# Performance work log

Measured on AMD Instinct MI355X. Metric: run time of the kernel, lower is better.

The kernel has to match this reference:

```python
import jax, jax.numpy as jnp
import numpy as np

B, T, S = 32, 64, 256
H, E, V = 512, 256, 32000
NH = 8
HD = H // NH  # 64
L = 2  # gru layers
SCALE = float(np.sqrt(HD))


def setup_inputs() -> dict:
    key = jax.random.key(0)
    ks = jax.random.split(key, 32)

    def rn(k, shape, s=0.02):
        return (jax.random.normal(k, shape) * s).astype(jnp.float32)

    inp = {}
    inp["tgt"] = jax.random.randint(ks[0], (B, T), 0, V)
    inp["encoder_out"] = jax.random.normal(ks[1], (B, S, H), dtype=jnp.float32)
    inp["decoder_init"] = jax.random.normal(ks[2], (B, H), dtype=jnp.float32)
    inp["src_mask"] = jnp.ones((B, S), dtype=jnp.int32)
    # parameters
    inp["emb_table"] = rn(ks[3], (V, E)).at[0].set(0.0)  # padding_idx=0
    inp["w_ep"] = rn(ks[4], (H, E)); inp["b_ep"] = jnp.zeros((H,), jnp.float32)
    inp["wq"] = rn(ks[5], (H, H)); inp["bq"] = jnp.zeros((H,), jnp.float32)
    inp["wk"] = rn(ks[6], (H, H)); inp["bk"] = jnp.zeros((H,), jnp.float32)
    inp["wv"] = rn(ks[7], (H, H)); inp["bv"] = jnp.zeros((H,), jnp.float32)
    inp["wo"] = rn(ks[8], (H, H)); inp["bo"] = jnp.zeros((H,), jnp.float32)
    # GRU layer 0: input 2H, layer 1: input H
    inp["w_ih0"] = rn(ks[9], (3 * H, 2 * H)); inp["w_hh0"] = rn(ks[10], (3 * H, H))
    inp["b_ih0"] = jnp.zeros((3 * H,), jnp.float32); inp["b_hh0"] = jnp.zeros((3 * H,), jnp.float32)
    inp["w_ih1"] = rn(ks[11], (3 * H, H)); inp["w_hh1"] = rn(ks[12], (3 * H, H))
    inp["b_ih1"] = jnp.zeros((3 * H,), jnp.float32); inp["b_hh1"] = jnp.zeros((3 * H,), jnp.float32)
    # output MLP
    inp["w_o1"] = rn(ks[13], (H, 2 * H)); inp["b_o1"] = jnp.zeros((H,), jnp.float32)
    inp["w_o2"] = rn(ks[14], (V, H)); inp["b_o2"] = jnp.zeros((V,), jnp.float32)
    return inp


def _gru_cell(x, h, w_ih, w_hh, b_ih, b_hh):
    gi = x @ w_ih.T + b_ih
    gh = h @ w_hh.T + b_hh
    i_r, i_z, i_n = jnp.split(gi, 3, axis=-1)
    h_r, h_z, h_n = jnp.split(gh, 3, axis=-1)
    r = jax.nn.sigmoid(i_r + h_r)
    z = jax.nn.sigmoid(i_z + h_z)
    n = jnp.tanh(i_n + r * h_n)
    return (1.0 - z) * n + z * h


def reference(tgt, encoder_out, decoder_init, src_mask,
              emb_table, w_ep, b_ep, wq, bq, wk, bk, wv, bv, wo, bo,
              w_ih0, w_hh0, b_ih0, b_hh0, w_ih1, w_hh1, b_ih1, b_hh1,
              w_o1, b_o1, w_o2, b_o2):
    # initial hidden: [L, B, H], clamped
    hidden0 = jnp.clip(jnp.broadcast_to(decoder_init[None], (L, B, H)), -10.0, 10.0)
    # K/V projections of encoder_out are step-invariant -> hoist out of the loop
    Kh = jnp.clip(encoder_out @ wk.T + bk, -100.0, 100.0).reshape(B, S, NH, HD)
    Vh = (encoder_out @ wv.T + bv).reshape(B, S, NH, HD)
    pad = (src_mask == 0)  # [B, S]

    def step(hidden, tok):
        emb = emb_table[tok] @ w_ep.T + b_ep                      # [B, H]
        q = jnp.clip(hidden[-1] @ wq.T + bq, -100.0, 100.0).reshape(B, NH, HD)
        scores = jnp.einsum('bhd,bshd->bhs', q, Kh) / SCALE       # [B, NH, S]
        scores = jnp.where(pad[:, None, :], -10000.0, scores)
        attn = jax.nn.softmax(scores, axis=-1)
        ctx = jnp.einsum('bhs,bshd->bhd', attn, Vh).reshape(B, H)
        ctx = jnp.clip(ctx @ wo.T + bo, -100.0, 100.0)            # [B, H]
        x = jnp.concatenate([emb, ctx], axis=1)                   # [B, 2H]
        h0 = _gru_cell(x, hidden[0], w_ih0, w_hh0, b_ih0, b_hh0)
        h1 = _gru_cell(h0, hidden[1], w_ih1, w_hh1, b_ih1, b_hh1)
        new_hidden = jnp.clip(jnp.stack([h0, h1]), -10.0, 10.0)
        comb = jnp.concatenate([h1, ctx], axis=1)                 # gru_out pre-clamp
        out = jax.nn.relu(comb @ w_o1.T + b_o1) @ w_o2.T + b_o2   # [B, V]
        return new_hidden, jnp.clip(out, -100.0, 100.0)

    # teacher forcing (tf_ratio = 1.0): input at step t is tgt[:, t-1]
    _, outs = jax.lax.scan(step, hidden0, tgt[:, :-1].T)          # [T-1, B, V]
    outputs = jnp.concatenate(
        [jnp.zeros((B, 1, V), outs.dtype), outs.transpose(1, 0, 2)], axis=1)
    return outputs
```

## Files before the change

kernel.cpp:

```cpp
#include <hip/hip_runtime.h>
#include <hip/hip_bf16.h>
#include <math.h>

#define B 32
#define T 64
#define S 256
#define H 512
#define E 256
#define V 32000
#define NH 8
#define HD 64
#define TS 63
#define NR 2016
#define G3 1536

typedef short bf16x8 __attribute__((ext_vector_type(8)));
typedef float f32x4 __attribute__((ext_vector_type(4)));

__device__ __forceinline__ unsigned short f2bf(float f) {
    union { float f; unsigned u; } v; v.f = f;
    unsigned r = v.u + 0x7FFF + ((v.u >> 16) & 1);
    return (unsigned short)(r >> 16);
}
__device__ __forceinline__ float clipf(float v, float lo, float hi) {
    return fminf(hi, fmaxf(lo, v));
}
__device__ __forceinline__ float sigf(float x) { return 1.0f / (1.0f + __expf(-x)); }

__device__ __forceinline__ void stA(float* p, float v) {
    __hip_atomic_store(p, v, __ATOMIC_RELAXED, __HIP_MEMORY_SCOPE_AGENT);
}
__device__ __forceinline__ unsigned long long ldA64(const void* p) {
    return __hip_atomic_load((const unsigned long long*)p, __ATOMIC_RELAXED, __HIP_MEMORY_SCOPE_AGENT);
}

#define XIDX(k) ((((k) >> 7) * 132) + ((k) & 127))
#define BLP 528


__global__ void k_zero_t0(float* out) {
    int idx = blockIdx.x * 256 + threadIdx.x;
    int n = B * V / 4;
    if (idx < n) {
        int b = idx / (V / 4);
        int v4 = idx % (V / 4);
        float4* p = (float4*)(out + (size_t)b * T * V) + v4;
        *p = make_float4(0.f, 0.f, 0.f, 0.f);
    }
}

__global__ void k_init_h(const float* dec, float* h0n, float* h1s) {
    int i = blockIdx.x * 256 + threadIdx.x;
    if (i < B * H) {
        float v = clipf(dec[i], -10.f, 10.f);
        h0n[16384 + i] = v;
        h1s[16384 + i] = v;
    }
}

__global__ __launch_bounds__(256) void k_kv(const float* __restrict__ enc,
        const float* __restrict__ wk, const float* __restrict__ bk,
        const float* __restrict__ wv, const float* __restrict__ bv,
        float* __restrict__ kht, float* __restrict__ vh) {
    __shared__ float x[8][512];
    int r0 = blockIdx.x * 8;
    for (int idx = threadIdx.x; idx < 4096; idx += 256) {
        int rr = idx >> 9, k = idx & 511;
        x[rr][k] = enc[(size_t)(r0 + rr) * 512 + k];
    }
    __syncthreads();
    int b = r0 >> 8, s0 = r0 & 255;
    for (int ii = 0; ii < 2; ++ii) {
        int i = threadIdx.x + ii * 256;
        const float* wkr = wk + (size_t)i * 512;
        const float* wvr = wv + (size_t)i * 512;
        float aK[8], aV[8];
        float bk0 = bk[i], bv0 = bv[i];
        #pragma unroll
        for (int rr = 0; rr < 8; ++rr) { aK[rr] = bk0; aV[rr] = bv0; }
        for (int k = 0; k < 512; k += 4) {
            float4 a = *(const float4*)(wkr + k);
            float4 c = *(const float4*)(wvr + k);
            #pragma unroll
            for (int rr = 0; rr < 8; ++rr) {
                float4 xv = *(const float4*)(&x[rr][k]);
                aK[rr] += a.x*xv.x + a.y*xv.y + a.z*xv.z + a.w*xv.w;
                aV[rr] += c.x*xv.x + c.y*xv.y + c.z*xv.z + c.w*xv.w;
            }
        }
        #pragma unroll
        for (int rr = 0; rr < 8; ++rr) {
            kht[((size_t)b * 512 + i) * 256 + s0 + rr] = clipf(aK[rr], -100.f, 100.f);
            vh[((size_t)b * 256 + s0 + rr) * 512 + i] = aV[rr];
        }
    }
}

__global__ __launch_bounds__(256) void k_gie(const int* __restrict__ tgt,
        const float* __restrict__ embt, const float* __restrict__ wep,
        const float* __restrict__ bep, const float* __restrict__ wih0,
        const float* __restrict__ bih0, float* __restrict__ gie) {
    __shared__ float er[8][256];
    __shared__ float xf[8][512];
    int r0 = blockIdx.x * 8;
    for (int idx = threadIdx.x; idx < 2048; idx += 256) {
        int rr = idx >> 8, k = idx & 255;
        int rw = r0 + rr; int tt = rw >> 5, bb = rw & 31;
        er[rr][k] = embt[(size_t)tgt[bb * T + tt] * 256 + k];
    }
    __syncthreads();
    for (int ii = 0; ii < 2; ++ii) {
        int i = threadIdx.x + ii * 256;
        const float* wr = wep + (size_t)i * 256;
        float acc[8];
        float b0 = bep[i];
        #pragma unroll
        for (int rr = 0; rr < 8; ++rr) acc[rr] = b0;
        for (int k = 0; k < 256; k += 4) {
            float4 w4 = *(const float4*)(wr + k);
            #pragma unroll
            for (int rr = 0; rr < 8; ++rr) {
                float4 xv = *(const float4*)(&er[rr][k]);
                acc[rr] += w4.x*xv.x + w4.y*xv.y + w4.z*xv.z + w4.w*xv.w;
            }
        }
        #pragma unroll
        for (int rr = 0; rr < 8; ++rr) xf[rr][i] = acc[rr];
    }
    __syncthreads();
    for (int jj = 0; jj < 6; ++jj) {
        int j = threadIdx.x + jj * 256;
        const float* wr = wih0 + (size_t)j * 1024;
        float acc[8];
        float b0 = bih0[j];
        #pragma unroll
        for (int rr = 0; rr < 8; ++rr) acc[rr] = b0;
        for (int k = 0; k < 512; k += 4) {
            float4 w4 = *(const float4*)(wr + k);
            #pragma unroll
            for (int rr = 0; rr < 8; ++rr) {
                float4 xv = *(const float4*)(&xf[rr][k]);
                acc[rr] += w4.x*xv.x + w4.y*xv.y + w4.z*xv.z + w4.w*xv.w;
            }
        }
        #pragma unroll
        for (int rr = 0; rr < 8; ++rr) gie[(size_t)(r0 + rr) * 1536 + j] = acc[rr];
    }
}

__global__ void k_cvt(const float* __restrict__ wo1, const float* __restrict__ wo2,
                      unsigned short* __restrict__ w1b, unsigned short* __restrict__ w2b) {
    size_t idx = (size_t)blockIdx.x * 256 + threadIdx.x;
    size_t stride = (size_t)gridDim.x * 256;
    size_t n1 = (size_t)H * 2 * H;
    size_t n2 = (size_t)V * H;
    for (size_t i = idx; i < n1; i += stride) w1b[i] = f2bf(wo1[i]);
    for (size_t i = idx; i < n2; i += stride) w2b[i] = f2bf(wo2[i]);
}


__device__ __forceinline__ void gbar(unsigned* c, unsigned target) {
    __syncthreads();
    if (threadIdx.x == 0) {
        asm volatile("s_waitcnt vmcnt(0)" ::: "memory");
        __hip_atomic_fetch_add(c, 1u, __ATOMIC_RELAXED, __HIP_MEMORY_SCOPE_AGENT);
        while (__hip_atomic_load(c, __ATOMIC_RELAXED, __HIP_MEMORY_SCOPE_AGENT) < target) {
            __builtin_amdgcn_s_sleep(1);
        }
    }
    __syncthreads();
}

__device__ __forceinline__ void stage4(float* dst, const float* src, bool doclip) {
    const unsigned long long* s = (const unsigned long long*)src;
    #pragma unroll
    for (int i = 0; i < 4; ++i) {
        int w = threadIdx.x + i * 256;
        union { unsigned long long u; float f[2]; } c;
        c.u = ldA64(s + w);
        int bl = w >> 8;
        int k = (w & 255) * 2;
        float a = c.f[0], b2 = c.f[1];
        if (doclip) { a = clipf(a, -10.f, 10.f); b2 = clipf(b2, -10.f, 10.f); }
        int base = bl * BLP + XIDX(k);
        dst[base] = a; dst[base + 1] = b2;
    }
}

__device__ __forceinline__ float dot128(const float* __restrict__ w, const float* x) {
    float acc = 0.f;
    #pragma unroll 8
    for (int k = 0; k < 128; k += 4) {
        float4 a = *(const float4*)(w + k);
        acc += a.x * x[k] + a.y * x[k+1] + a.z * x[k+2] + a.w * x[k+3];
    }
    return acc;
}

__global__ __launch_bounds__(256, 1) void k_rec(
        const float* __restrict__ kht, const float* __restrict__ vh,
        const float* __restrict__ gie, const int* __restrict__ maskp,
        const float* __restrict__ wq,  const float* __restrict__ bq,
        const float* __restrict__ wo,  const float* __restrict__ bo,
        const float* __restrict__ wih0, const float* __restrict__ whh0, const float* __restrict__ bhh0,
        const float* __restrict__ wih1, const float* __restrict__ bih1,
        const float* __restrict__ whh1, const float* __restrict__ bhh1,
        float* __restrict__ ctx, float* __restrict__ ctxo,
        float* __restrict__ h0n, float* __restrict__ h1s,
        unsigned short* __restrict__ comb, unsigned* bar) {
    __shared__ float SA[4 * BLP];
    __shared__ float SB[4 * BLP];
    __shared__ float pq[256];
    __shared__ float qv[64];
    __shared__ float sc[256];
    __shared__ float cp[256];
    __shared__ float red[8];

    const int tid = threadIdx.x;
    const int wgid = blockIdx.x;
    const int grp = wgid >> 5;
    const int w = wgid & 31;
    const int bg0 = grp * 4;
    const int ab = bg0 + (w >> 3);
    const int ah = w & 7;
    const int jb = w * 16;
    const int bl = tid >> 6;
    const int lane = tid & 63;
    const int r = lane & 15;
    const int p4 = lane >> 4;
    const int bg = bg0 + bl;
    const bool fin = (lane < 16);
    const int wid = tid >> 6;
    const bool apad = (maskp[ab * S + tid] == 0);
    unsigned* barp = bar + grp * 64;
    unsigned bcount = 0;

    for (int t = 0; t < TS; ++t) {
        const int par = t & 1;
        const float* h1rd = h1s + (par ^ 1) * 16384;
        float* h1wr = h1s + par * 16384;
        const float* h0rd = h0n + (par ^ 1) * 16384;
        float* h0wr = h0n + par * 16384;

        {
            union { unsigned long long u; float f[2]; } c;
            c.u = ldA64((const unsigned long long*)(h1rd + ab * 512) + tid);
            int k2 = tid * 2;
            SA[XIDX(k2)]     = clipf(c.f[0], -10.f, 10.f);
            SA[XIDX(k2) + 1] = clipf(c.f[1], -10.f, 10.f);
        }
        __syncthreads();
        {
            int f = tid >> 2, p = tid & 3;
            pq[f * 4 + p] = dot128(wq + (size_t)(ah * 64 + f) * 512 + p * 128, SA + p * 132);
        }
        __syncthreads();
        if (tid < 64)
            qv[tid] = clipf(pq[tid*4] + pq[tid*4+1] + pq[tid*4+2] + pq[tid*4+3]
                            + bq[ah * 64 + tid], -100.f, 100.f);
        __syncthreads();
        {
            const float* kr = kht + ((size_t)ab * 512 + ah * 64) * 256 + tid;
            float acc = 0.f;
            #pragma unroll 8
            for (int d = 0; d < 64; ++d) acc += qv[d] * kr[(size_t)d * 256];
            sc[tid] = apad ? -10000.f : acc * 0.125f;
        }
        __syncthreads();
        {
            float v = sc[tid];
            float m = v;
            for (int o = 32; o >= 1; o >>= 1) m = fmaxf(m, __shfl_xor(m, o, 64));
            if ((tid & 63) == 0) red[wid] = m;
            __syncthreads();
            m = fmaxf(fmaxf(red[0], red[1]), fmaxf(red[2], red[3]));
            float e = __expf(v - m);
            float s = e;
            for (int o = 32; o >= 1; o >>= 1) s += __shfl_xor(s, o, 64);
            if ((tid & 63) == 0) red[4 + wid] = s;
            __syncthreads();
            float inv = 1.f / (red[4] + red[5] + red[6] + red[7]);
            sc[tid] = e * inv;
        }
        __syncthreads();
        {
            const float* vr = vh + ((size_t)ab * 256 + (tid >> 6) * 64) * 512 + ah * 64 + (tid & 63);
            float acc = 0.f;
            #pragma unroll 4
            for (int s2 = 0; s2 < 64; ++s2) acc += sc[(tid >> 6) * 64 + s2] * vr[(size_t)s2 * 512];
            cp[tid] = acc;
        }
        __syncthreads();
        if (tid < 64)
            stA(&ctx[ab * 512 + ah * 64 + tid],
                cp[tid] + cp[64 + tid] + cp[128 + tid] + cp[192 + tid]);
        gbar(barp, (++bcount) * 32);

        stage4(SA, ctx + bg0 * 512, false);
        __syncthreads();
        {
            float a = dot128(wo + (size_t)(jb + r) * 512 + p4 * 128, SA + bl * BLP + p4 * 132);
            a += __shfl_xor(a, 16, 64);
            a += __shfl_xor(a, 32, 64);
            if (fin) {
                int j = jb + r;
                float v = clipf(a + bo[j], -100.f, 100.f);
                stA(&ctxo[bg * 512 + j], v);
                comb[(size_t)(t * 32 + bg) * 1024 + 512 + j] = f2bf(v);
            }
        }
        gbar(barp, (++bcount) * 32);

        stage4(SA, ctxo + bg0 * 512, false);
        stage4(SB, h0rd + bg0 * 512, true);
        __syncthreads();
        float gi3[3], gh3[3];
        #pragma unroll
        for (int g3 = 0; g3 < 3; ++g3) {
            int row = g3 * 512 + jb + r;
            float gi = dot128(wih0 + (size_t)row * 1024 + 512 + p4 * 128, SA + bl * BLP + p4 * 132);
            float gh = dot128(whh0 + (size_t)row * 512 + p4 * 128, SB + bl * BLP + p4 * 132);
            gi += __shfl_xor(gi, 16, 64); gi += __shfl_xor(gi, 32, 64);
            gh += __shfl_xor(gh, 16, 64); gh += __shfl_xor(gh, 32, 64);
            gi3[g3] = gi; gh3[g3] = gh;
        }
        if (fin) {
            int j = jb + r;
            const float* gp = gie + (size_t)(t * 32 + bg) * 1536;
            float gir = gi3[0] + gp[j];
            float giz = gi3[1] + gp[512 + j];
            float gin = gi3[2] + gp[1024 + j];
            float ghr = gh3[0] + bhh0[j];
            float ghz = gh3[1] + bhh0[512 + j];
            float ghn = gh3[2] + bhh0[1024 + j];
            float r_ = sigf(gir + ghr);
            float z_ = sigf(giz + ghz);
            float n_ = tanhf(gin + r_ * ghn);
            float h0old = SB[bl * BLP + XIDX(j)];
            float hn = (1.f - z_) * n_ + z_ * h0old;
            stA(&h0wr[bg * 512 + j], hn);
        }
        gbar(barp, (++bcount) * 32);

        stage4(SA, h0wr + bg0 * 512, false);
        stage4(SB, h1rd + bg0 * 512, true);
        __syncthreads();
        #pragma unroll
        for (int g3 = 0; g3 < 3; ++g3) {
            int row = g3 * 512 + jb + r;
            float gi = dot128(wih1 + (size_t)row * 512 + p4 * 128, SA + bl * BLP + p4 * 132);
            float gh = dot128(whh1 + (size_t)row * 512 + p4 * 128, SB + bl * BLP + p4 * 132);
            gi += __shfl_xor(gi, 16, 64); gi += __shfl_xor(gi, 32, 64);
            gh += __shfl_xor(gh, 16, 64); gh += __shfl_xor(gh, 32, 64);
            gi3[g3] = gi; gh3[g3] = gh;
        }
        if (fin) {
            int j = jb + r;
            float gir = gi3[0] + bih1[j];
            float giz = gi3[1] + bih1[512 + j];
            float gin = gi3[2] + bih1[1024 + j];
            float ghr = gh3[0] + bhh1[j];
            float ghz = gh3[1] + bhh1[512 + j];
            float ghn = gh3[2] + bhh1[1024 + j];
            float r_ = sigf(gir + ghr);
            float z_ = sigf(giz + ghz);
            float n_ = tanhf(gin + r_ * ghn);
            float h1old = SB[bl * BLP + XIDX(j)];
            float hn = (1.f - z_) * n_ + z_ * h1old;
            stA(&h1wr[bg * 512 + j], hn);
            comb[(size_t)(t * 32 + bg) * 1024 + j] = f2bf(hn);
        }
        gbar(barp, (++bcount) * 32);
    }
}

template<int K, int EPI>
__global__ __launch_bounds__(256) void k_gemm(const unsigned short* __restrict__ A,
        const unsigned short* __restrict__ Bm, const float* __restrict__ bias,
        void* __restrict__ outp) {
    __shared__ unsigned short As[128][72];
    __shared__ unsigned short Bs[128][72];
    const int tid = threadIdx.x;
    const int wave = tid >> 6, lane = tid & 63;
    const int wm = wave >> 1, wn = wave & 1;
    const int m0 = blockIdx.y * 128, n0 = blockIdx.x * 128;
    const int m16 = lane & 15, q = lane >> 4;
    f32x4 acc[4][4];
    #pragma unroll
    for (int i = 0; i < 4; ++i)
        #pragma unroll
        for (int j = 0; j < 4; ++j) acc[i][j] = (f32x4){0.f, 0.f, 0.f, 0.f};

    for (int k0 = 0; k0 < K; k0 += 64) {
        __syncthreads();
        #pragma unroll
        for (int i = 0; i < 4; ++i) {
            int c = tid + i * 256;
            int row = c >> 3, c8 = c & 7;
            int ar = m0 + row; if (ar > NR - 1) ar = NR - 1;
            *(bf16x8*)&As[row][c8 * 8] = *(const bf16x8*)(A + (size_t)ar * K + k0 + c8 * 8);
            *(bf16x8*)&Bs[row][c8 * 8] = *(const bf16x8*)(Bm + (size_t)(n0 + row) * K + k0 + c8 * 8);
        }
        __syncthreads();
        #pragma unroll
        for (int kk = 0; kk < 64; kk += 32) {
            bf16x8 af[4], bfr[4];
            #pragma unroll
            for (int mi = 0; mi < 4; ++mi)
                af[mi] = *(const bf16x8*)&As[wm * 64 + mi * 16 + m16][kk + q * 8];
            #pragma unroll
            for (int ni = 0; ni < 4; ++ni)
                bfr[ni] = *(const bf16x8*)&Bs[wn * 64 + ni * 16 + m16][kk + q * 8];
            #pragma unroll
            for (int mi = 0; mi < 4; ++mi)
                #pragma unroll
                for (int ni = 0; ni < 4; ++ni)
                    acc[mi][ni] = __builtin_amdgcn_mfma_f32_16x16x32_bf16(af[mi], bfr[ni], acc[mi][ni], 0, 0, 0);
        }
    }
    #pragma unroll
    for (int mi = 0; mi < 4; ++mi)
        #pragma unroll
        for (int ni = 0; ni < 4; ++ni) {
            int n = n0 + wn * 64 + ni * 16 + m16;
            float bv = bias[n];
            #pragma unroll
            for (int rg = 0; rg < 4; ++rg) {
                int row = m0 + wm * 64 + mi * 16 + q * 4 + rg;
                if (row < NR) {
                    float v = acc[mi][ni][rg] + bv;
                    if (EPI == 0) {
                        v = fmaxf(v, 0.f);
                        ((unsigned short*)outp)[(size_t)row * 512 + n] = f2bf(v);
                    } else {
                        int tt = row >> 5, bb = row & 31;
                        v = clipf(v, -100.f, 100.f);
                        ((float*)outp)[(size_t)bb * T * V + (size_t)(tt + 1) * V + n] = v;
                    }
                }
            }
        }
}


extern "C" void kernel_launch(void* const* d_in, const int* in_sizes, int n_in,
                              void* d_out, int out_size, void* d_ws, size_t ws_size,
                              hipStream_t stream) {
    const int*   tgt  = (const int*)d_in[0];
    const float* enc  = (const float*)d_in[1];
    const float* dec  = (const float*)d_in[2];
    const int*   mask = (const int*)d_in[3];
    const float* embt = (const float*)d_in[4];
    const float* wep  = (const float*)d_in[5];  const float* bep = (const float*)d_in[6];
    const float* wq   = (const float*)d_in[7];  const float* bq  = (const float*)d_in[8];
    const float* wk   = (const float*)d_in[9];  const float* bk  = (const float*)d_in[10];
    const float* wv   = (const float*)d_in[11]; const float* bv  = (const float*)d_in[12];
    const float* wo   = (const float*)d_in[13]; const float* bo  = (const float*)d_in[14];
    const float* wih0 = (const float*)d_in[15]; const float* whh0 = (const float*)d_in[16];
    const float* bih0 = (const float*)d_in[17]; const float* bhh0 = (const float*)d_in[18];
    const float* wih1 = (const float*)d_in[19]; const float* whh1 = (const float*)d_in[20];
    const float* bih1 = (const float*)d_in[21]; const float* bhh1 = (const float*)d_in[22];
    const float* wo1  = (const float*)d_in[23]; const float* bo1 = (const float*)d_in[24];
    const float* wo2  = (const float*)d_in[25]; const float* bo2 = (const float*)d_in[26];
    float* out = (float*)d_out;
    char* ws = (char*)d_ws;

    float* kht           = (float*)(ws + 0);
    float* vh            = (float*)(ws + 16777216);
    float* gie           = (float*)(ws + 33554432);
    unsigned short* comb = (unsigned short*)(ws + 45940736);
    unsigned short* h1b  = (unsigned short*)(ws + 50069504);
    unsigned short* w1b  = (unsigned short*)(ws + 52133888);
    unsigned short* w2b  = (unsigned short*)(ws + 53182464);
    float* ctx           = (float*)(ws + 85950464);
    float* ctxo          = (float*)(ws + 86016000);
    float* h0n           = (float*)(ws + 86081536);
    float* h1s           = (float*)(ws + 86212608);
    unsigned* bar        = (unsigned*)(ws + 86343680);

    hipMemsetAsync(bar, 0, 4096, stream);
    hipLaunchKernelGGL(k_zero_t0, dim3(1000), dim3(256), 0, stream, out);
    hipLaunchKernelGGL(k_init_h, dim3(64), dim3(256), 0, stream, dec, h0n, h1s);
    hipLaunchKernelGGL(k_kv, dim3(B * S / 8), dim3(256), 0, stream, enc, wk, bk, wv, bv, kht, vh);
    hipLaunchKernelGGL(k_gie, dim3(NR / 8), dim3(256), 0, stream, tgt, embt, wep, bep, wih0, bih0, gie);
    hipLaunchKernelGGL(k_cvt, dim3(4096), dim3(256), 0, stream, wo1, wo2, w1b, w2b);
    hipLaunchKernelGGL(k_rec, dim3(256), dim3(256), 0, stream,
                       kht, vh, gie, mask, wq, bq, wo, bo,
                       wih0, whh0, bhh0, wih1, bih1, whh1, bhh1,
                       ctx, ctxo, h0n, h1s, comb, bar);
    hipLaunchKernelGGL(HIP_KERNEL_NAME(k_gemm<1024, 0>), dim3(4, 16), dim3(256), 0, stream,
                       comb, w1b, bo1, (void*)h1b);
    hipLaunchKernelGGL(HIP_KERNEL_NAME(k_gemm<512, 1>), dim3(250, 16), dim3(256), 0, stream,
                       h1b, w2b, bo2, (void*)out);
}
```

Baseline: 5.884 ms.

## Cache per-head K/V in LDS for recurrence and keep W2 tile resident in output GEMM

The recurrent kernel now loads each workgroup's K and V head slices (64x256 floats each) into shared memory once before the time loop, replacing 63 steps of global reads. The output-projection GEMM becomes a 250-block kernel where each block holds its full 128x512 W2 slice in LDS and loops over all 16 M tiles, so W2 is read once instead of 16 times. The cost is much larger LDS use (about 128 KB in the recurrence, about 150 KB in the GEMM), which limits occupancy. It also leaves only 250 workgroups with serialized M tiles and no overlap between loads and MFMA.

```diff
diff --git a/kernel.cpp b/kernel.cpp
--- a/kernel.cpp
+++ b/kernel.cpp
@@ -208,6 +208,8 @@
         float* __restrict__ ctx, float* __restrict__ ctxo,
         float* __restrict__ h0n, float* __restrict__ h1s,
         unsigned short* __restrict__ comb, unsigned* bar) {
+    __shared__ float Kl[64][256];
+    __shared__ float Vl[256][64];
     __shared__ float SA[4 * BLP];
     __shared__ float SB[4 * BLP];
     __shared__ float pq[256];
@@ -235,6 +237,20 @@
     unsigned* barp = bar + grp * 64;
     unsigned bcount = 0;
 
+    {
+        const float4* kb = (const float4*)(kht + ((size_t)ab * 512 + ah * 64) * 256);
+        float4* kl = (float4*)&Kl[0][0];
+        #pragma unroll
+        for (int i = tid; i < 4096; i += 256) kl[i] = kb[i];
+        #pragma unroll
+        for (int i = tid; i < 4096; i += 256) {
+            int s = i >> 4, dc = i & 15;
+            float4 vv = *(const float4*)(vh + ((size_t)ab * 256 + s) * 512 + ah * 64 + dc * 4);
+            *(float4*)&Vl[s][dc * 4] = vv;
+        }
+    }
+    __syncthreads();
+
     for (int t = 0; t < TS; ++t) {
         const int par = t & 1;
         const float* h1rd = h1s + (par ^ 1) * 16384;
@@ -260,10 +276,9 @@
                             + bq[ah * 64 + tid], -100.f, 100.f);
         __syncthreads();
         {
-            const float* kr = kht + ((size_t)ab * 512 + ah * 64) * 256 + tid;
             float acc = 0.f;
             #pragma unroll 8
-            for (int d = 0; d < 64; ++d) acc += qv[d] * kr[(size_t)d * 256];
+            for (int d = 0; d < 64; ++d) acc += qv[d] * Kl[d][tid];
             sc[tid] = apad ? -10000.f : acc * 0.125f;
         }
         __syncthreads();
@@ -284,10 +299,10 @@
         }
         __syncthreads();
         {
-            const float* vr = vh + ((size_t)ab * 256 + (tid >> 6) * 64) * 512 + ah * 64 + (tid & 63);
+            int d = tid & 63, cch = tid >> 6;
             float acc = 0.f;
             #pragma unroll 4
-            for (int s2 = 0; s2 < 64; ++s2) acc += sc[(tid >> 6) * 64 + s2] * vr[(size_t)s2 * 512];
+            for (int s2 = 0; s2 < 64; ++s2) acc += sc[cch * 64 + s2] * Vl[cch * 64 + s2][d];
             cp[tid] = acc;
         }
         __syncthreads();
@@ -374,10 +389,9 @@
     }
 }
 
-template<int K, int EPI>
-__global__ __launch_bounds__(256) void k_gemm(const unsigned short* __restrict__ A,
+__global__ __launch_bounds__(256) void k_g1(const unsigned short* __restrict__ A,
         const unsigned short* __restrict__ Bm, const float* __restrict__ bias,
-        void* __restrict__ outp) {
+        unsigned short* __restrict__ outp) {
     __shared__ unsigned short As[128][72];
     __shared__ unsigned short Bs[128][72];
     const int tid = threadIdx.x;
@@ -391,15 +405,15 @@
         #pragma unroll
         for (int j = 0; j < 4; ++j) acc[i][j] = (f32x4){0.f, 0.f, 0.f, 0.f};
 
-    for (int k0 = 0; k0 < K; k0 += 64) {
+    for (int k0 = 0; k0 < 1024; k0 += 64) {
         __syncthreads();
         #pragma unroll
         for (int i = 0; i < 4; ++i) {
             int c = tid + i * 256;
             int row = c >> 3, c8 = c & 7;
             int ar = m0 + row; if (ar > NR - 1) ar = NR - 1;
-            *(bf16x8*)&As[row][c8 * 8] = *(const bf16x8*)(A + (size_t)ar * K + k0 + c8 * 8);
-            *(bf16x8*)&Bs[row][c8 * 8] = *(const bf16x8*)(Bm + (size_t)(n0 + row) * K + k0 + c8 * 8);
+            *(bf16x8*)&As[row][c8 * 8] = *(const bf16x8*)(A + (size_t)ar * 1024 + k0 + c8 * 8);
+            *(bf16x8*)&Bs[row][c8 * 8] = *(const bf16x8*)(Bm + (size_t)(n0 + row) * 1024 + k0 + c8 * 8);
         }
         __syncthreads();
         #pragma unroll
@@ -428,18 +442,80 @@
             for (int rg = 0; rg < 4; ++rg) {
                 int row = m0 + wm * 64 + mi * 16 + q * 4 + rg;
                 if (row < NR) {
-                    float v = acc[mi][ni][rg] + bv;
-                    if (EPI == 0) {
-                        v = fmaxf(v, 0.f);
-                        ((unsigned short*)outp)[(size_t)row * 512 + n] = f2bf(v);
-                    } else {
+                    float v = fmaxf(acc[mi][ni][rg] + bv, 0.f);
+                    outp[(size_t)row * 512 + n] = f2bf(v);
+                }
+            }
+        }
+}
+
+__global__ __launch_bounds__(256, 1) void k_g2(const unsigned short* __restrict__ h1b,
+        const unsigned short* __restrict__ w2b, const float* __restrict__ b2,
+        float* __restrict__ out) {
+    __shared__ unsigned short Bs[128][520];
+    __shared__ unsigned short As[128][72];
+    const int tid = threadIdx.x;
+    const int wave = tid >> 6, lane = tid & 63;
+    const int wm = wave >> 1, wn = wave & 1;
+    const int n0 = blockIdx.x * 128;
+    const int m16 = lane & 15, q = lane >> 4;
+
+    for (int i = tid; i < 128 * 64; i += 256) {
+        int row = i >> 6, c8 = i & 63;
+        *(bf16x8*)&Bs[row][c8 * 8] = *(const bf16x8*)(w2b + (size_t)(n0 + row) * 512 + c8 * 8);
+    }
+
+    for (int mt = 0; mt < 16; ++mt) {
+        int m0 = mt * 128;
+        f32x4 acc[4][4];
+        #pragma unroll
+        for (int i = 0; i < 4; ++i)
+            #pragma unroll
+            for (int j = 0; j < 4; ++j) acc[i][j] = (f32x4){0.f, 0.f, 0.f, 0.f};
+
+        for (int k0 = 0; k0 < 512; k0 += 64) {
+            __syncthreads();
+            #pragma unroll
+            for (int i = 0; i < 4; ++i) {
+                int c = tid + i * 256;
+                int row = c >> 3, c8 = c & 7;
+                int ar = m0 + row; if (ar > NR - 1) ar = NR - 1;
+                *(bf16x8*)&As[row][c8 * 8] = *(const bf16x8*)(h1b + (size_t)ar * 512 + k0 + c8 * 8);
+            }
+            __syncthreads();
+            #pragma unroll
+            for (int kk = 0; kk < 64; kk += 32) {
+                bf16x8 af[4], bfr[4];
+                #pragma unroll
+                for (int mi = 0; mi < 4; ++mi)
+                    af[mi] = *(const bf16x8*)&As[wm * 64 + mi * 16 + m16][kk + q * 8];
+                #pragma unroll
+                for (int ni = 0; ni < 4; ++ni)
+                    bfr[ni] = *(const bf16x8*)&Bs[wn * 64 + ni * 16 + m16][k0 + kk + q * 8];
+                #pragma unroll
+                for (int mi = 0; mi < 4; ++mi)
+                    #pragma unroll
+                    for (int ni = 0; ni < 4; ++ni)
+                        acc[mi][ni] = __builtin_amdgcn_mfma_f32_16x16x32_bf16(af[mi], bfr[ni], acc[mi][ni], 0, 0, 0);
+            }
+        }
+        #pragma unroll
+        for (int mi = 0; mi < 4; ++mi)
+            #pragma unroll
+            for (int ni = 0; ni < 4; ++ni) {
+                int n = n0 + wn * 64 + ni * 16 + m16;
+                float bv = b2[n];
+                #pragma unroll
+                for (int rg = 0; rg < 4; ++rg) {
+                    int row = m0 + wm * 64 + mi * 16 + q * 4 + rg;
+                    if (row < NR) {
                         int tt = row >> 5, bb = row & 31;
-                        v = clipf(v, -100.f, 100.f);
-                        ((float*)outp)[(size_t)bb * T * V + (size_t)(tt + 1) * V + n] = v;
+                        float v = clipf(acc[mi][ni][rg] + bv, -100.f, 100.f);
+                        out[(size_t)bb * T * V + (size_t)(tt + 1) * V + n] = v;
                     }
                 }
             }
-        }
+    }
 }
 
 
@@ -488,8 +564,6 @@
                        kht, vh, gie, mask, wq, bq, wo, bo,
                        wih0, whh0, bhh0, wih1, bih1, whh1, bhh1,
                        ctx, ctxo, h0n, h1s, comb, bar);
-    hipLaunchKernelGGL(HIP_KERNEL_NAME(k_gemm<1024, 0>), dim3(4, 16), dim3(256), 0, stream,
-                       comb, w1b, bo1, (void*)h1b);
-    hipLaunchKernelGGL(HIP_KERNEL_NAME(k_gemm<512, 1>), dim3(250, 16), dim3(256), 0, stream,
-                       h1b, w2b, bo2, (void*)out);
-}
+    hipLaunchKernelGGL(k_g1, dim3(4, 16), dim3(256), 0, stream, comb, w1b, bo1, h1b);
+    hipLaunchKernelGGL(k_g2, dim3(250), dim3(256), 0, stream, h1b, w2b, bo2, out);
+}
```

Result: faster. 5.193 ms (-11.7%).
